# Kernel optimization log

Hardware: AMD Instinct MI355X
Metric: run time of the kernel (lower is better)

Reference implementation:

```python
import jax, jax.numpy as jnp
import numpy as np
import math

EMBED_DIM = 128
NUM_HEADS = 8
HEAD_DIM = EMBED_DIM // NUM_HEADS
# Faithful to the source's concat bug: heads [0,1,1,2,3,4,5,6] (head 7 dropped, head 1 duplicated)
HEAD_ORDER = [0, 1, 1, 2, 3, 4, 5, 6]


def setup_inputs() -> dict:
    key = jax.random.key(0)
    ks = jax.random.split(key, 7)
    B, S = 4, 2048
    input_embeddings = jax.random.normal(ks[0], (B, S, EMBED_DIM), dtype=jnp.float32)
    token_attention_masks = jax.random.randint(ks[1], (B, S), 0, 2, dtype=jnp.int64)
    # torch.rand -> uniform [0,1)
    w_query = jax.random.uniform(ks[2], (EMBED_DIM, EMBED_DIM), dtype=jnp.float32)
    w_key = jax.random.uniform(ks[3], (EMBED_DIM, EMBED_DIM), dtype=jnp.float32)
    w_value = jax.random.uniform(ks[4], (EMBED_DIM, EMBED_DIM), dtype=jnp.float32)
    # nn.Linear params
    lim = 1.0 / math.sqrt(EMBED_DIM)
    lin_w = jax.random.uniform(ks[5], (EMBED_DIM, EMBED_DIM), dtype=jnp.float32, minval=-lim, maxval=lim)
    lin_b = jax.random.uniform(ks[6], (EMBED_DIM,), dtype=jnp.float32, minval=-lim, maxval=lim)
    return {"input_embeddings": input_embeddings, "token_attention_masks": token_attention_masks,
            "w_query": w_query, "w_key": w_key, "w_value": w_value, "lin_w": lin_w, "lin_b": lin_b}


def reference(input_embeddings, token_attention_masks, w_query, w_key, w_value, lin_w, lin_b):
    B, S, _ = input_embeddings.shape
    q = input_embeddings @ w_query  # [B,S,D]
    k = input_embeddings @ w_key
    v = input_embeddings @ w_value
    # split heads: [B,S,H,hd] -> [B,H,S,hd]
    qh = q.reshape(B, S, NUM_HEADS, HEAD_DIM).transpose(0, 2, 1, 3)
    kh = k.reshape(B, S, NUM_HEADS, HEAD_DIM).transpose(0, 2, 1, 3)
    vh = v.reshape(B, S, NUM_HEADS, HEAD_DIM).transpose(0, 2, 1, 3)
    # NOTE: source scales by sqrt(full embedding dim), not sqrt(head_dim)
    scale = 1.0 / math.sqrt(EMBED_DIM)
    scores = jnp.einsum('bhsd,bhtd->bhst', qh, kh) * scale  # [B,H,S,S]
    # mask: 0 -> -1000, 1 -> 0; broadcast over query positions
    mask = jnp.where(token_attention_masks == 0, -1000.0, 0.0).astype(scores.dtype)  # [B,S]
    scores = scores + mask[:, None, None, :]
    probs = jax.nn.softmax(scores, axis=-1)
    out_h = jnp.einsum('bhst,bhtd->bhsd', probs, vh)  # [B,H,S,hd]
    # buggy concat order kept faithful
    attn_out = jnp.concatenate([out_h[:, i] for i in HEAD_ORDER], axis=-1)  # [B,S,D]
    return attn_out @ lin_w.T + lin_b
```

## Files before the change

kernel.cpp:

```cpp
#include <hip/hip_runtime.h>
#include <stdint.h>

typedef unsigned short u16;
typedef unsigned int   u32;
typedef float   f32x4  __attribute__((ext_vector_type(4)));
typedef float   f32x16 __attribute__((ext_vector_type(16)));
typedef __bf16  bf16x8 __attribute__((ext_vector_type(8)));
typedef u32     u32x4  __attribute__((ext_vector_type(4)));
typedef u32     u32x2  __attribute__((ext_vector_type(2)));

union BF8 { bf16x8 v; u16 s[8]; u32x4 q; };

__device__ __forceinline__ u16 f2b_rne(float f) {
    u32 u = __builtin_bit_cast(u32, f);
    u32 r = u + 0x7FFFu + ((u >> 16) & 1u);
    return (u16)(r >> 16);
}
__device__ __forceinline__ u16 f2b_trunc(float f) {
    return (u16)(__builtin_bit_cast(u32, f) >> 16);
}
__device__ __forceinline__ float b2f(u16 h) {
    u32 u = ((u32)h) << 16;
    return __builtin_bit_cast(float, u);
}
__device__ __forceinline__ bf16x8 ld_bf8(const u16* p) {
    BF8 t; t.q = *(const u32x4*)p; return t.v;
}
__device__ __forceinline__ f32x16 zero16() {
    f32x16 z;
#pragma unroll
    for (int i = 0; i < 16; i++) z[i] = 0.f;
    return z;
}
__device__ __forceinline__ f32x4 zero4() {
    f32x4 z;
#pragma unroll
    for (int i = 0; i < 4; i++) z[i] = 0.f;
    return z;
}

#define SCALE2 0.1275312959479341f
#define MBIAS2 -1442.6950408889634f

__global__ __launch_bounds__(256) void proj_kernel(
    const float* __restrict__ x, const float* __restrict__ wq,
    const float* __restrict__ wk, const float* __restrict__ wv,
    u16* Qph, u16* Qpl, u16* Kph, u16* Kpl, u16* VT)
{
    int typ  = blockIdx.y;
    int ct   = threadIdx.x >> 6;
    int lane = threadIdx.x & 63;
    int m = lane & 31, kg = lane >> 5;
    int r0 = blockIdx.x * 32;
    int c = ct * 32 + m;

    const float* wp = (typ == 0) ? wq : (typ == 1) ? wk : wv;

    f32x16 acc = zero16();
    for (int kk = 0; kk < 128; kk += 16) {
        const float* xp = x + (size_t)(r0 + m) * 128 + kk + kg * 8;
        f32x4 x0 = *(const f32x4*)xp;
        f32x4 x1 = *(const f32x4*)(xp + 4);
        BF8 ah, al;
#pragma unroll
        for (int j = 0; j < 4; j++) {
            u16 hb = f2b_trunc(x0[j]);
            ah.s[j] = hb; al.s[j] = f2b_trunc(x0[j] - b2f(hb));
            u16 hb2 = f2b_trunc(x1[j]);
            ah.s[4 + j] = hb2; al.s[4 + j] = f2b_trunc(x1[j] - b2f(hb2));
        }
        const float* wcol = wp + (size_t)(kk + kg * 8) * 128 + c;
        if (typ < 2) {
            BF8 bh, bl_;
#pragma unroll
            for (int j = 0; j < 8; j++) {
                float w = wcol[(size_t)j * 128];
                u16 hb = f2b_trunc(w);
                bh.s[j] = hb; bl_.s[j] = f2b_trunc(w - b2f(hb));
            }
            acc = __builtin_amdgcn_mfma_f32_32x32x16_bf16(ah.v, bh.v, acc, 0, 0, 0);
            acc = __builtin_amdgcn_mfma_f32_32x32x16_bf16(ah.v, bl_.v, acc, 0, 0, 0);
            acc = __builtin_amdgcn_mfma_f32_32x32x16_bf16(al.v, bh.v, acc, 0, 0, 0);
        } else {
            BF8 bh;
#pragma unroll
            for (int j = 0; j < 8; j++) bh.s[j] = f2b_rne(wcol[(size_t)j * 128]);
            acc = __builtin_amdgcn_mfma_f32_32x32x16_bf16(ah.v, bh.v, acc, 0, 0, 0);
        }
    }

    int b = r0 >> 11, sl = r0 & 2047;
    if (typ < 2) {
        u16* H = typ ? Kph : Qph;
        u16* L = typ ? Kpl : Qpl;
        int hh = c >> 4, d = c & 15;
        if (hh == 7) return;
        float scl = (typ == 0) ? SCALE2 : 1.0f;
        size_t hb_off = (size_t)(b * 8 + hh) * 2048 * 16 + d;
#pragma unroll
        for (int r = 0; r < 16; r++) {
            int row = (r & 3) + 8 * (r >> 2) + 4 * kg;
            float v = acc[r] * scl;
            u16 hi = f2b_trunc(v);
            size_t idx = hb_off + (size_t)(sl + row) * 16;
            H[idx] = hi;
            L[idx] = f2b_trunc(v - b2f(hi));
        }
    } else {
        if ((c >> 4) == 7) return;
#pragma unroll
        for (int rg = 0; rg < 4; rg++) {
            int rowb = rg * 8 + 4 * kg;
            BF8 pk;
#pragma unroll
            for (int q = 0; q < 4; q++) pk.s[q] = f2b_rne(acc[rg * 4 + q]);
            u32x4 tmp = pk.q;
            *(u32*)(VT + (size_t)(b * 128 + c) * 2048 + sl + rowb)     = tmp[0];
            *(u32*)(VT + (size_t)(b * 128 + c) * 2048 + sl + rowb + 2) = tmp[1];
        }
    }
}

__global__ __launch_bounds__(256, 6) void attn_kernel(
    const u16* __restrict__ Qph, const u16* __restrict__ Qpl,
    const u16* __restrict__ Kph, const u16* __restrict__ Kpl,
    const u16* __restrict__ VT, const int* __restrict__ mask, u16* AO)
{
    __shared__ char smem[18944];
    u16*   pbuf  = (u16*)smem;
    float* biasC = (float*)(smem + 10240);
    float* lsmax = (float*)(smem + 18432);
    float* obuf  = (float*)smem;
    float* lbuf  = (float*)(smem + 8192);

    int bid = blockIdx.x;
    int bh = bid % 28;
    int qt = bid / 28;
    int b = bh / 7, h = bh % 7;
    int wave = threadIdx.x >> 6, lane = threadIdx.x & 63;
    int m = lane & 31, kg = lane >> 5;
    int qs = qt * 32;

    {
        int e0 = threadIdx.x * 8;
        const int* mp = mask + b * 2048;
        float v[8];
#pragma unroll
        for (int j = 0; j < 8; j++) {
            int e = e0 + j;
            int ti = e >> 5, kgg = (e >> 4) & 1, r = e & 15;
            int key = ti * 32 + (r & 3) + 8 * (r >> 2) + 4 * kgg;
            v[j] = (mp[key] != 0) ? 0.0f : MBIAS2;
        }
        *(f32x4*)(biasC + e0)     = *(const f32x4*)&v[0];
        *(f32x4*)(biasC + e0 + 4) = *(const f32x4*)&v[4];
    }
    __syncthreads();

    size_t headoff = (size_t)(b * 8 + h) * 2048 * 16;
    bf16x8 qfh = ld_bf8(Qph + headoff + (size_t)(qs + m) * 16 + kg * 8);
    bf16x8 qfl = ld_bf8(Qpl + headoff + (size_t)(qs + m) * 16 + kg * 8);
    const u16* kbh = Kph + headoff;
    const u16* kbl = Kpl + headoff;

    int t0 = wave * 512;

    float mloc = -3.0e38f;
    for (int t = t0; t < t0 + 512; t += 32) {
        bf16x8 kh8 = ld_bf8(kbh + (size_t)(t + m) * 16 + kg * 8);
        f32x16 ci = *(const f32x16*)(biasC + (t >> 5) * 32 + kg * 16);
        f32x16 sc = __builtin_amdgcn_mfma_f32_32x32x16_bf16(kh8, qfh, ci, 0, 0, 0);
#pragma unroll
        for (int r = 0; r < 16; r++) mloc = fmaxf(mloc, sc[r]);
    }
    mloc = fmaxf(mloc, __shfl_xor(mloc, 32, 64));
    if (kg == 0) lsmax[m * 4 + wave] = mloc;
    __syncthreads();
    f32x4 mv = *(const f32x4*)(lsmax + m * 4);
    float mrow = fmaxf(fmaxf(mv[0], mv[1]), fmaxf(mv[2], mv[3]));

    f32x4 o0 = zero4(), o1 = zero4(), l0 = zero4(), l1 = zero4();
    BF8 onesu;
#pragma unroll
    for (int j = 0; j < 8; j++) onesu.s[j] = 0x3F80;
    bf16x8 ones = onesu.v;

    int q16 = lane & 15, krow = lane >> 4;
    const u16* vtb = VT + (size_t)(b * 128 + h * 16 + q16) * 2048;
    u16* pw = pbuf + wave * 1280 + m * 40 + kg * 4;
    const u16* pr0 = pbuf + wave * 1280 + q16 * 40 + krow * 8;
    const u16* pr1 = pr0 + 16 * 40;

    for (int t = t0; t < t0 + 512; t += 32) {
        bf16x8 kh8 = ld_bf8(kbh + (size_t)(t + m) * 16 + kg * 8);
        bf16x8 kl8 = ld_bf8(kbl + (size_t)(t + m) * 16 + kg * 8);
        f32x16 ci = *(const f32x16*)(biasC + (t >> 5) * 32 + kg * 16);
        f32x16 sc = __builtin_amdgcn_mfma_f32_32x32x16_bf16(kh8, qfl, ci, 0, 0, 0);
        sc = __builtin_amdgcn_mfma_f32_32x32x16_bf16(kl8, qfh, sc, 0, 0, 0);
        sc = __builtin_amdgcn_mfma_f32_32x32x16_bf16(kh8, qfh, sc, 0, 0, 0);
#pragma unroll
        for (int rg = 0; rg < 4; rg++) {
            float e0 = __builtin_amdgcn_exp2f(sc[rg * 4 + 0] - mrow);
            float e1 = __builtin_amdgcn_exp2f(sc[rg * 4 + 1] - mrow);
            float e2 = __builtin_amdgcn_exp2f(sc[rg * 4 + 2] - mrow);
            float e3 = __builtin_amdgcn_exp2f(sc[rg * 4 + 3] - mrow);
            u32x2 pk;
            pk[0] = __builtin_amdgcn_perm(__builtin_bit_cast(u32, e1),
                                          __builtin_bit_cast(u32, e0), 0x07060302u);
            pk[1] = __builtin_amdgcn_perm(__builtin_bit_cast(u32, e3),
                                          __builtin_bit_cast(u32, e2), 0x07060302u);
            *(u32x2*)(pw + rg * 8) = pk;
        }
        bf16x8 vf = ld_bf8(vtb + t + krow * 8);
        bf16x8 p0 = *(const bf16x8*)pr0;
        bf16x8 p1 = *(const bf16x8*)pr1;
        o0 = __builtin_amdgcn_mfma_f32_16x16x32_bf16(p0, vf, o0, 0, 0, 0);
        o1 = __builtin_amdgcn_mfma_f32_16x16x32_bf16(p1, vf, o1, 0, 0, 0);
        l0 = __builtin_amdgcn_mfma_f32_16x16x32_bf16(p0, ones, l0, 0, 0, 0);
        l1 = __builtin_amdgcn_mfma_f32_16x16x32_bf16(p1, ones, l1, 0, 0, 0);
    }

    __syncthreads();

    *(f32x4*)(obuf + wave * 512 + q16 * 32 + krow * 4)      = o0;
    *(f32x4*)(obuf + wave * 512 + q16 * 32 + krow * 4 + 16) = o1;
    if (q16 == 0) {
        *(f32x4*)(lbuf + wave * 32 + krow * 4)      = l0;
        *(f32x4*)(lbuf + wave * 32 + krow * 4 + 16) = l1;
    }
    __syncthreads();

    int dd = threadIdx.x & 15, q = threadIdx.x >> 4;
    int slot0 = (h == 0) ? 0 : h + 1;
#pragma unroll
    for (int hf = 0; hf < 2; hf++) {
        int qq = q + hf * 16;
        float os = obuf[0 * 512 + dd * 32 + qq] + obuf[1 * 512 + dd * 32 + qq]
                 + obuf[2 * 512 + dd * 32 + qq] + obuf[3 * 512 + dd * 32 + qq];
        float ls = lbuf[0 * 32 + qq] + lbuf[1 * 32 + qq]
                 + lbuf[2 * 32 + qq] + lbuf[3 * 32 + qq];
        u16 vb = f2b_rne(os * __builtin_amdgcn_rcpf(ls));
        int orow = b * 2048 + qs + qq;
        AO[orow * 128 + slot0 * 16 + dd] = vb;
        if (h == 1) AO[orow * 128 + 16 + dd] = vb;
    }
}

__global__ __launch_bounds__(256) void fin_kernel(
    const u16* __restrict__ AO, const float* __restrict__ lw,
    const float* __restrict__ lb, float* out)
{
    int ct   = threadIdx.x >> 6;
    int lane = threadIdx.x & 63;
    int m = lane & 31, kg = lane >> 5;
    int r0 = blockIdx.x * 32;
    int c = ct * 32 + m;

    f32x16 acc = zero16();
    for (int kk = 0; kk < 128; kk += 16) {
        bf16x8 af = ld_bf8(AO + (size_t)(r0 + m) * 128 + kk + kg * 8);
        const float* wp = lw + (size_t)c * 128 + kk + kg * 8;
        f32x4 w0 = *(const f32x4*)wp;
        f32x4 w1 = *(const f32x4*)(wp + 4);
        BF8 bfr;
#pragma unroll
        for (int j = 0; j < 4; j++) {
            bfr.s[j]     = f2b_rne(w0[j]);
            bfr.s[4 + j] = f2b_rne(w1[j]);
        }
        acc = __builtin_amdgcn_mfma_f32_32x32x16_bf16(af, bfr.v, acc, 0, 0, 0);
    }
    float bias = lb[c];
#pragma unroll
    for (int r = 0; r < 16; r++) {
        int row = (r & 3) + 8 * (r >> 2) + 4 * kg;
        out[(size_t)(r0 + row) * 128 + c] = acc[r] + bias;
    }
}

extern "C" void kernel_launch(void* const* d_in, const int* in_sizes, int n_in,
                              void* d_out, int out_size, void* d_ws, size_t ws_size,
                              hipStream_t stream)
{
    const float* x    = (const float*)d_in[0];
    const int*   mask = (const int*)d_in[1];
    const float* wq   = (const float*)d_in[2];
    const float* wk   = (const float*)d_in[3];
    const float* wv   = (const float*)d_in[4];
    const float* lw   = (const float*)d_in[5];
    const float* lb   = (const float*)d_in[6];
    float* out = (float*)d_out;

    char* ws = (char*)d_ws;
    u16* Qph = (u16*)(ws + 0 * 2097152);
    u16* Qpl = (u16*)(ws + 1 * 2097152);
    u16* Kph = (u16*)(ws + 2 * 2097152);
    u16* Kpl = (u16*)(ws + 3 * 2097152);
    u16* VT  = (u16*)(ws + 4 * 2097152);
    u16* AO  = (u16*)(ws + 5 * 2097152);

    proj_kernel<<<dim3(256, 3), 256, 0, stream>>>(x, wq, wk, wv,
                                                  Qph, Qpl, Kph, Kpl, VT);
    attn_kernel<<<1792, 256, 0, stream>>>(Qph, Qpl, Kph, Kpl, VT, mask, AO);
    fin_kernel<<<256, 256, 0, stream>>>(AO, lw, lb, out);
}
```

Baseline: 125.9 us.

## Pre-transpose inputs, transpose attention output, prefetch K tiles, shrink LDS padding

A new kernel pre-splits x into transposed bf16 hi/lo planes and transposes the output linear weight to bf16, so the projection and final kernels read bf16 directly without per-block conversion. The attention kernel now software-prefetches the next K tile in both passes, hoists the V load earlier, shrinks the P buffer row stride from 40 to 34 to cut LDS and raise occupancy to 7, and writes its output transposed. The cost is an extra kernel launch plus more workspace traffic. The transposed layouts also turn proj/fin operand loads into strided scalar 16-bit loads, and the odd LDS stride may cause bank conflicts.

```diff
diff --git a/kernel.cpp b/kernel.cpp
--- a/kernel.cpp
+++ b/kernel.cpp
@@ -42,9 +42,50 @@
 #define SCALE2 0.1275312959479341f
 #define MBIAS2 -1442.6950408889634f
 
+__global__ __launch_bounds__(256) void xt_kernel(
+    const float* __restrict__ x, const float* __restrict__ lw,
+    u16* XTh, u16* XTl, u16* lwT)
+{
+    __shared__ float xs[32][65];
+    int t = threadIdx.x;
+    if (blockIdx.x < 512) {
+        int ts = blockIdx.x & 127, td = blockIdx.x >> 7;
+        int r0 = ts * 64, d0 = td * 32;
+        int ci = t & 31, ro = t >> 5;
+#pragma unroll
+        for (int j = 0; j < 8; j++)
+            xs[ci][ro + 8 * j] = x[(size_t)(r0 + ro + 8 * j) * 128 + d0 + ci];
+        __syncthreads();
+        int ri = t & 63, dj = t >> 6;
+#pragma unroll
+        for (int jj = 0; jj < 8; jj++) {
+            int di = dj + 4 * jj;
+            float v = xs[di][ri];
+            u16 hi = f2b_trunc(v);
+            XTh[(size_t)(d0 + di) * 8192 + r0 + ri] = hi;
+            XTl[(size_t)(d0 + di) * 8192 + r0 + ri] = f2b_trunc(v - b2f(hi));
+        }
+    } else {
+        int tb = blockIdx.x - 512;
+        int to = (tb & 1) * 64, ti = (tb >> 1) * 32;
+        int ci = t & 31, ro = t >> 5;
+#pragma unroll
+        for (int j = 0; j < 8; j++)
+            xs[ci][ro + 8 * j] = lw[(size_t)(to + ro + 8 * j) * 128 + ti + ci];
+        __syncthreads();
+        int oi = t & 63, dj = t >> 6;
+#pragma unroll
+        for (int jj = 0; jj < 8; jj++) {
+            int ii = dj + 4 * jj;
+            lwT[(size_t)(ti + ii) * 128 + to + oi] = f2b_rne(xs[ii][oi]);
+        }
+    }
+}
+
 __global__ __launch_bounds__(256) void proj_kernel(
-    const float* __restrict__ x, const float* __restrict__ wq,
-    const float* __restrict__ wk, const float* __restrict__ wv,
+    const u16* __restrict__ XTh, const u16* __restrict__ XTl,
+    const float* __restrict__ wq, const float* __restrict__ wk,
+    const float* __restrict__ wv,
     u16* Qph, u16* Qpl, u16* Kph, u16* Kpl, u16* VT)
 {
     int typ  = blockIdx.y;
@@ -57,20 +98,18 @@
     const float* wp = (typ == 0) ? wq : (typ == 1) ? wk : wv;
 
     f32x16 acc = zero16();
+#pragma unroll 4
     for (int kk = 0; kk < 128; kk += 16) {
-        const float* xp = x + (size_t)(r0 + m) * 128 + kk + kg * 8;
-        f32x4 x0 = *(const f32x4*)xp;
-        f32x4 x1 = *(const f32x4*)(xp + 4);
-        BF8 ah, al;
-#pragma unroll
-        for (int j = 0; j < 4; j++) {
-            u16 hb = f2b_trunc(x0[j]);
-            ah.s[j] = hb; al.s[j] = f2b_trunc(x0[j] - b2f(hb));
-            u16 hb2 = f2b_trunc(x1[j]);
-            ah.s[4 + j] = hb2; al.s[4 + j] = f2b_trunc(x1[j] - b2f(hb2));
-        }
+        const u16* xh = XTh + (size_t)(kk + kg * 8) * 8192 + r0 + m;
+        BF8 ah;
+#pragma unroll
+        for (int j = 0; j < 8; j++) ah.s[j] = xh[(size_t)j * 8192];
         const float* wcol = wp + (size_t)(kk + kg * 8) * 128 + c;
         if (typ < 2) {
+            const u16* xl = XTl + (size_t)(kk + kg * 8) * 8192 + r0 + m;
+            BF8 al;
+#pragma unroll
+            for (int j = 0; j < 8; j++) al.s[j] = xl[(size_t)j * 8192];
             BF8 bh, bl_;
 #pragma unroll
             for (int j = 0; j < 8; j++) {
@@ -121,15 +160,15 @@
     }
 }
 
-__global__ __launch_bounds__(256, 6) void attn_kernel(
+__global__ __launch_bounds__(256, 7) void attn_kernel(
     const u16* __restrict__ Qph, const u16* __restrict__ Qpl,
     const u16* __restrict__ Kph, const u16* __restrict__ Kpl,
-    const u16* __restrict__ VT, const int* __restrict__ mask, u16* AO)
-{
-    __shared__ char smem[18944];
+    const u16* __restrict__ VT, const int* __restrict__ mask, u16* AOT)
+{
+    __shared__ char smem[17408];
     u16*   pbuf  = (u16*)smem;
-    float* biasC = (float*)(smem + 10240);
-    float* lsmax = (float*)(smem + 18432);
+    float* biasC = (float*)(smem + 8704);
+    float* lsmax = (float*)(smem + 16896);
     float* obuf  = (float*)smem;
     float* lbuf  = (float*)(smem + 8192);
 
@@ -166,12 +205,17 @@
     int t0 = wave * 512;
 
     float mloc = -3.0e38f;
-    for (int t = t0; t < t0 + 512; t += 32) {
-        bf16x8 kh8 = ld_bf8(kbh + (size_t)(t + m) * 16 + kg * 8);
-        f32x16 ci = *(const f32x16*)(biasC + (t >> 5) * 32 + kg * 16);
-        f32x16 sc = __builtin_amdgcn_mfma_f32_32x32x16_bf16(kh8, qfh, ci, 0, 0, 0);
-#pragma unroll
-        for (int r = 0; r < 16; r++) mloc = fmaxf(mloc, sc[r]);
+    {
+        bf16x8 khc = ld_bf8(kbh + (size_t)(t0 + m) * 16 + kg * 8);
+        for (int t = t0; t < t0 + 512; t += 32) {
+            int tn = (t + 32 < t0 + 512) ? (t + 32) : t0;
+            bf16x8 khn = ld_bf8(kbh + (size_t)(tn + m) * 16 + kg * 8);
+            f32x16 ci = *(const f32x16*)(biasC + (t >> 5) * 32 + kg * 16);
+            f32x16 sc = __builtin_amdgcn_mfma_f32_32x32x16_bf16(khc, qfh, ci, 0, 0, 0);
+#pragma unroll
+            for (int r = 0; r < 16; r++) mloc = fmaxf(mloc, sc[r]);
+            khc = khn;
+        }
     }
     mloc = fmaxf(mloc, __shfl_xor(mloc, 32, 64));
     if (kg == 0) lsmax[m * 4 + wave] = mloc;
@@ -187,17 +231,23 @@
 
     int q16 = lane & 15, krow = lane >> 4;
     const u16* vtb = VT + (size_t)(b * 128 + h * 16 + q16) * 2048;
-    u16* pw = pbuf + wave * 1280 + m * 40 + kg * 4;
-    const u16* pr0 = pbuf + wave * 1280 + q16 * 40 + krow * 8;
-    const u16* pr1 = pr0 + 16 * 40;
+    u16* pw = pbuf + wave * 1088 + m * 34 + kg * 4;
+    const u16* pr0 = pbuf + wave * 1088 + q16 * 34 + krow * 8;
+    const u16* pr1 = pr0 + 16 * 34;
+
+    bf16x8 khc = ld_bf8(kbh + (size_t)(t0 + m) * 16 + kg * 8);
+    bf16x8 klc = ld_bf8(kbl + (size_t)(t0 + m) * 16 + kg * 8);
 
     for (int t = t0; t < t0 + 512; t += 32) {
-        bf16x8 kh8 = ld_bf8(kbh + (size_t)(t + m) * 16 + kg * 8);
-        bf16x8 kl8 = ld_bf8(kbl + (size_t)(t + m) * 16 + kg * 8);
-        f32x16 ci = *(const f32x16*)(biasC + (t >> 5) * 32 + kg * 16);
-        f32x16 sc = __builtin_amdgcn_mfma_f32_32x32x16_bf16(kh8, qfl, ci, 0, 0, 0);
-        sc = __builtin_amdgcn_mfma_f32_32x32x16_bf16(kl8, qfh, sc, 0, 0, 0);
-        sc = __builtin_amdgcn_mfma_f32_32x32x16_bf16(kh8, qfh, sc, 0, 0, 0);
+        int tn = (t + 32 < t0 + 512) ? (t + 32) : t0;
+        bf16x8 khn = ld_bf8(kbh + (size_t)(tn + m) * 16 + kg * 8);
+        bf16x8 kln = ld_bf8(kbl + (size_t)(tn + m) * 16 + kg * 8);
+        bf16x8 vf  = ld_bf8(vtb + t + krow * 8);
+
+        f32x16 sc = *(const f32x16*)(biasC + (t >> 5) * 32 + kg * 16);
+        sc = __builtin_amdgcn_mfma_f32_32x32x16_bf16(khc, qfl, sc, 0, 0, 0);
+        sc = __builtin_amdgcn_mfma_f32_32x32x16_bf16(klc, qfh, sc, 0, 0, 0);
+        sc = __builtin_amdgcn_mfma_f32_32x32x16_bf16(khc, qfh, sc, 0, 0, 0);
 #pragma unroll
         for (int rg = 0; rg < 4; rg++) {
             float e0 = __builtin_amdgcn_exp2f(sc[rg * 4 + 0] - mrow);
@@ -211,13 +261,13 @@
                                           __builtin_bit_cast(u32, e2), 0x07060302u);
             *(u32x2*)(pw + rg * 8) = pk;
         }
-        bf16x8 vf = ld_bf8(vtb + t + krow * 8);
         bf16x8 p0 = *(const bf16x8*)pr0;
         bf16x8 p1 = *(const bf16x8*)pr1;
         o0 = __builtin_amdgcn_mfma_f32_16x16x32_bf16(p0, vf, o0, 0, 0, 0);
         o1 = __builtin_amdgcn_mfma_f32_16x16x32_bf16(p1, vf, o1, 0, 0, 0);
         l0 = __builtin_amdgcn_mfma_f32_16x16x32_bf16(p0, ones, l0, 0, 0, 0);
         l1 = __builtin_amdgcn_mfma_f32_16x16x32_bf16(p1, ones, l1, 0, 0, 0);
+        khc = khn; klc = kln;
     }
 
     __syncthreads();
@@ -241,13 +291,13 @@
                  + lbuf[2 * 32 + qq] + lbuf[3 * 32 + qq];
         u16 vb = f2b_rne(os * __builtin_amdgcn_rcpf(ls));
         int orow = b * 2048 + qs + qq;
-        AO[orow * 128 + slot0 * 16 + dd] = vb;
-        if (h == 1) AO[orow * 128 + 16 + dd] = vb;
+        AOT[(size_t)(slot0 * 16 + dd) * 8192 + orow] = vb;
+        if (h == 1) AOT[(size_t)(16 + dd) * 8192 + orow] = vb;
     }
 }
 
 __global__ __launch_bounds__(256) void fin_kernel(
-    const u16* __restrict__ AO, const float* __restrict__ lw,
+    const u16* __restrict__ AOT, const u16* __restrict__ lwT,
     const float* __restrict__ lb, float* out)
 {
     int ct   = threadIdx.x >> 6;
@@ -257,18 +307,17 @@
     int c = ct * 32 + m;
 
     f32x16 acc = zero16();
+#pragma unroll 4
     for (int kk = 0; kk < 128; kk += 16) {
-        bf16x8 af = ld_bf8(AO + (size_t)(r0 + m) * 128 + kk + kg * 8);
-        const float* wp = lw + (size_t)c * 128 + kk + kg * 8;
-        f32x4 w0 = *(const f32x4*)wp;
-        f32x4 w1 = *(const f32x4*)(wp + 4);
-        BF8 bfr;
-#pragma unroll
-        for (int j = 0; j < 4; j++) {
-            bfr.s[j]     = f2b_rne(w0[j]);
-            bfr.s[4 + j] = f2b_rne(w1[j]);
-        }
-        acc = __builtin_amdgcn_mfma_f32_32x32x16_bf16(af, bfr.v, acc, 0, 0, 0);
+        BF8 af, bfr;
+        const u16* ap = AOT + (size_t)(kk + kg * 8) * 8192 + r0 + m;
+        const u16* bp = lwT + (size_t)(kk + kg * 8) * 128 + c;
+#pragma unroll
+        for (int j = 0; j < 8; j++) {
+            af.s[j]  = ap[(size_t)j * 8192];
+            bfr.s[j] = bp[(size_t)j * 128];
+        }
+        acc = __builtin_amdgcn_mfma_f32_32x32x16_bf16(af.v, bfr.v, acc, 0, 0, 0);
     }
     float bias = lb[c];
 #pragma unroll
@@ -292,15 +341,19 @@
     float* out = (float*)d_out;
 
     char* ws = (char*)d_ws;
-    u16* Qph = (u16*)(ws + 0 * 2097152);
-    u16* Qpl = (u16*)(ws + 1 * 2097152);
-    u16* Kph = (u16*)(ws + 2 * 2097152);
-    u16* Kpl = (u16*)(ws + 3 * 2097152);
-    u16* VT  = (u16*)(ws + 4 * 2097152);
-    u16* AO  = (u16*)(ws + 5 * 2097152);
-
-    proj_kernel<<<dim3(256, 3), 256, 0, stream>>>(x, wq, wk, wv,
+    u16* XTh = (u16*)(ws + 0 * 2097152);
+    u16* XTl = (u16*)(ws + 1 * 2097152);
+    u16* Qph = (u16*)(ws + 2 * 2097152);
+    u16* Qpl = (u16*)(ws + 3 * 2097152);
+    u16* Kph = (u16*)(ws + 4 * 2097152);
+    u16* Kpl = (u16*)(ws + 5 * 2097152);
+    u16* VT  = (u16*)(ws + 6 * 2097152);
+    u16* lwT = (u16*)(ws + 7 * 2097152);
+    u16* AOT = XTh;
+
+    xt_kernel<<<520, 256, 0, stream>>>(x, lw, XTh, XTl, lwT);
+    proj_kernel<<<dim3(256, 3), 256, 0, stream>>>(XTh, XTl, wq, wk, wv,
                                                   Qph, Qpl, Kph, Kpl, VT);
-    attn_kernel<<<1792, 256, 0, stream>>>(Qph, Qpl, Kph, Kpl, VT, mask, AO);
-    fin_kernel<<<256, 256, 0, stream>>>(AO, lw, lb, out);
-}
+    attn_kernel<<<1792, 256, 0, stream>>>(Qph, Qpl, Kph, Kpl, VT, mask, AOT);
+    fin_kernel<<<256, 256, 0, stream>>>(AOT, lwT, lb, out);
+}
```

Measured after the change: 182.9 us. 1.45x slower.
